# Optimization experiments

Measured on AMD Instinct MI355X. Metric: run time of the kernel, lower is better.

## Reference

```python
import jax, jax.numpy as jnp
import numpy as np

NUM_LAYERS = 3


def setup_inputs() -> dict:
    key = jax.random.key(0)
    k1, k2 = jax.random.split(key)
    N = 200000          # num_users + num_items
    D = 64              # latent_dim
    E = 4000000         # number of directed edges
    edge_index = jax.random.randint(k1, (2, E), 0, N, dtype=jnp.int64)
    emb_weight = 0.1 * jax.random.normal(k2, (N, D), dtype=jnp.float32)  # nn.init.normal_(std=0.1)
    return {"edge_index": edge_index, "emb_weight": emb_weight}


def reference(edge_index, emb_weight):
    N, D = emb_weight.shape
    src, dst = edge_index[0], edge_index[1]
    # gcn_norm (no self loops), as used by LGConv
    deg = jax.ops.segment_sum(jnp.ones_like(src, dtype=emb_weight.dtype), dst, num_segments=N)
    dinv = jnp.where(deg > 0, jax.lax.rsqrt(jnp.maximum(deg, 1.0)), 0.0)
    norm = dinv[src] * dinv[dst]            # [E]
    emb0 = emb_weight
    emb = emb0
    acc = emb0                              # running sum over layer embeddings
    for _ in range(NUM_LAYERS):
        msgs = norm[:, None] * emb[src]     # [E, D] irregular gather
        emb = jax.ops.segment_sum(msgs, dst, num_segments=N)  # scatter-add aggregate
        acc = acc + emb
    out = acc / (NUM_LAYERS + 1)            # mean over stacked layer embeddings
    return (emb0, out)
```

## Files before the change

kernel.cpp:

```cpp
#include <hip/hip_runtime.h>
#include <hip/hip_fp16.h>

#define DIM 64
#define BNODE_SHIFT 8
#define BNODE (1 << BNODE_SHIFT)
#define MAXNB 1024
#define BCAP_SHIFT 13
#define BCAP (1 << BCAP_SHIFT)
#define BIN_CHUNK 4096

__device__ inline __half2 as_h2(unsigned int u) {
    union { unsigned int u; __half2 h; } x; x.u = u; return x.h;
}
__device__ inline unsigned int as_u32(__half2 h) {
    union { unsigned int u; __half2 h; } x; x.h = h; return x.u;
}

__global__ void init_cursor_kernel(int* __restrict__ cursor, int NB) {
    int b = blockIdx.x * blockDim.x + threadIdx.x;
    if (b < NB) cursor[b] = b << BCAP_SHIFT;
}

__global__ void bin_kernel(const int* __restrict__ src, const int* __restrict__ dst,
                           int* __restrict__ cursor, unsigned int* __restrict__ packed,
                           int E, int NB) {
    __shared__ int lhist[MAXNB];
    __shared__ int lbase[MAXNB];
    const int t = threadIdx.x;
    for (int i = t; i < MAXNB; i += blockDim.x) lhist[i] = 0;
    __syncthreads();
    const long long beg = (long long)blockIdx.x * BIN_CHUNK;
    for (int j = 0; j < BIN_CHUNK / 256; ++j) {
        long long idx = beg + j * 256 + t;
        if (idx < E) atomicAdd(&lhist[dst[idx] >> BNODE_SHIFT], 1);
    }
    __syncthreads();
    for (int b = t; b < NB; b += blockDim.x) {
        int c = lhist[b];
        lbase[b] = c ? atomicAdd(&cursor[b], c) : 0;
    }
    __syncthreads();
    for (int i = t; i < MAXNB; i += blockDim.x) lhist[i] = 0;
    __syncthreads();
    for (int j = 0; j < BIN_CHUNK / 256; ++j) {
        long long idx = beg + j * 256 + t;
        if (idx < E) {
            int d = dst[idx];
            int b = d >> BNODE_SHIFT;
            int lpos = atomicAdd(&lhist[b], 1);
            packed[lbase[b] + lpos] =
                (unsigned int)src[idx] | ((unsigned int)(d & (BNODE - 1)) << 18);
        }
    }
}

__global__ void __launch_bounds__(BNODE) csr_kernel(
        const int* __restrict__ cursor, const unsigned int* __restrict__ packed,
        int* __restrict__ csr_src, float* __restrict__ dinv,
        int4* __restrict__ desc, int N) {
    __shared__ int hist[BNODE];
    __shared__ int s[BNODE];
    const int t = threadIdx.x;
    const int b = blockIdx.x;
    const int b0 = b << BCAP_SHIFT;
    const int cnt = cursor[b] - b0;
    hist[t] = 0;
    __syncthreads();
    for (int i = t; i < cnt; i += BNODE)
        atomicAdd(&hist[packed[b0 + i] >> 18], 1);
    __syncthreads();
    s[t] = hist[t];
    __syncthreads();
    for (int off = 1; off < BNODE; off <<= 1) {
        int v = s[t];
        int a = (t >= off) ? s[t - off] : 0;
        __syncthreads();
        s[t] = v + a;
        __syncthreads();
    }
    const int deg = hist[t];
    const int excl = s[t] - deg;
    const int myBeg = b0 + excl;
    const int node = (b << BNODE_SHIFT) + t;
    if (node < N) {
        float fd = (float)deg;
        float di2 = deg > 0 ? 1.0f / fd : 0.0f;
        dinv[node] = deg > 0 ? rsqrtf(fd) : 0.0f;
        desc[node] = make_int4(myBeg, myBeg + deg, deg, __float_as_int(di2));
    }
    __syncthreads();
    s[t] = excl;
    __syncthreads();
    for (int i = t; i < cnt; i += BNODE) {
        unsigned int p = packed[b0 + i];
        int lpos = atomicAdd(&s[p >> 18], 1);
        csr_src[b0 + lpos] = (int)(p & 0x3FFFFu);
    }
}

__global__ void conv0_kernel(const float* __restrict__ emb0, const float* __restrict__ dinv,
                             float* __restrict__ out_emb0, unsigned int* __restrict__ S0,
                             int n4) {
    int i = blockIdx.x * blockDim.x + threadIdx.x;
    if (i >= n4) return;
    float4 v = ((const float4*)emb0)[i];
    ((float4*)out_emb0)[i] = v;
    float w = dinv[i >> 4];
    uint2 o;
    o.x = as_u32(__float22half2_rn(make_float2(w * v.x, w * v.y)));
    o.y = as_u32(__float22half2_rn(make_float2(w * v.z, w * v.w)));
    ((uint2*)S0)[i] = o;
}

template<bool LAST>
__global__ void gather_kernel(const int4* __restrict__ desc,
                              const int* __restrict__ csr_src,
                              const unsigned int* __restrict__ S_in,
                              unsigned int* __restrict__ S_out,
                              const unsigned int* __restrict__ S1,
                              const float* __restrict__ emb0,
                              float* __restrict__ acc,
                              int N) {
    const int node = (blockIdx.x * blockDim.x + threadIdx.x) >> 6;
    if (node >= N) return;
    const int lane = threadIdx.x & 63;
    const int eg = lane >> 3;
    const int q  = lane & 7;
    const int4 d = desc[node];
    const int end = d.y;
    __half2 a0 = as_h2(0u), a1 = as_h2(0u), a2 = as_h2(0u), a3 = as_h2(0u);
    int i = d.x + eg;
    for (; i + 8 < end; i += 16) {
        int s0 = csr_src[i];
        int s1 = csr_src[i + 8];
        uint4 g0 = *(const uint4*)(S_in + (size_t)s0 * (DIM / 2) + q * 4);
        uint4 g1 = *(const uint4*)(S_in + (size_t)s1 * (DIM / 2) + q * 4);
        a0 = __hadd2(a0, as_h2(g0.x)); a1 = __hadd2(a1, as_h2(g0.y));
        a2 = __hadd2(a2, as_h2(g0.z)); a3 = __hadd2(a3, as_h2(g0.w));
        a0 = __hadd2(a0, as_h2(g1.x)); a1 = __hadd2(a1, as_h2(g1.y));
        a2 = __hadd2(a2, as_h2(g1.z)); a3 = __hadd2(a3, as_h2(g1.w));
    }
    if (i < end) {
        int s0 = csr_src[i];
        uint4 g0 = *(const uint4*)(S_in + (size_t)s0 * (DIM / 2) + q * 4);
        a0 = __hadd2(a0, as_h2(g0.x)); a1 = __hadd2(a1, as_h2(g0.y));
        a2 = __hadd2(a2, as_h2(g0.z)); a3 = __hadd2(a3, as_h2(g0.w));
    }
    #pragma unroll
    for (int m = 8; m < 64; m <<= 1) {
        a0 = __hadd2(a0, as_h2(__shfl_xor(as_u32(a0), m, 64)));
        a1 = __hadd2(a1, as_h2(__shfl_xor(as_u32(a1), m, 64)));
        a2 = __hadd2(a2, as_h2(__shfl_xor(as_u32(a2), m, 64)));
        a3 = __hadd2(a3, as_h2(__shfl_xor(as_u32(a3), m, 64)));
    }
    if (lane >= 8) return;
    const float di2 = __int_as_float(d.w);
    float2 f0 = __half22float2(a0);
    float2 f1 = __half22float2(a1);
    float2 f2 = __half22float2(a2);
    float2 f3 = __half22float2(a3);
    if (!LAST) {
        uint4 o;
        o.x = as_u32(__float22half2_rn(make_float2(di2 * f0.x, di2 * f0.y)));
        o.y = as_u32(__float22half2_rn(make_float2(di2 * f1.x, di2 * f1.y)));
        o.z = as_u32(__float22half2_rn(make_float2(di2 * f2.x, di2 * f2.y)));
        o.w = as_u32(__float22half2_rn(make_float2(di2 * f3.x, di2 * f3.y)));
        *(uint4*)(S_out + (size_t)node * (DIM / 2) + lane * 4) = o;
    } else {
        float rs = di2 > 0.f ? rsqrtf(di2) : 0.f;
        float dv = sqrtf(di2);
        uint4 u1 = *(const uint4*)(S1   + (size_t)node * (DIM / 2) + lane * 4);
        uint4 u2 = *(const uint4*)(S_in + (size_t)node * (DIM / 2) + lane * 4);
        float2 b0 = __half22float2(as_h2(u1.x)), c0 = __half22float2(as_h2(u2.x));
        float2 b1 = __half22float2(as_h2(u1.y)), c1 = __half22float2(as_h2(u2.y));
        float2 b2 = __half22float2(as_h2(u1.z)), c2 = __half22float2(as_h2(u2.z));
        float2 b3 = __half22float2(as_h2(u1.w)), c3 = __half22float2(as_h2(u2.w));
        const float* e = emb0 + (size_t)node * DIM + lane * 8;
        float4 e0 = *(const float4*)(e);
        float4 e1 = *(const float4*)(e + 4);
        float4 o0, o1;
        o0.x = 0.25f * (e0.x + rs * (b0.x + c0.x) + dv * f0.x);
        o0.y = 0.25f * (e0.y + rs * (b0.y + c0.y) + dv * f0.y);
        o0.z = 0.25f * (e0.z + rs * (b1.x + c1.x) + dv * f1.x);
        o0.w = 0.25f * (e0.w + rs * (b1.y + c1.y) + dv * f1.y);
        o1.x = 0.25f * (e1.x + rs * (b2.x + c2.x) + dv * f2.x);
        o1.y = 0.25f * (e1.y + rs * (b2.y + c2.y) + dv * f2.y);
        o1.z = 0.25f * (e1.z + rs * (b3.x + c3.x) + dv * f3.x);
        o1.w = 0.25f * (e1.w + rs * (b3.y + c3.y) + dv * f3.y);
        float* ap = acc + (size_t)node * DIM + lane * 8;
        *(float4*)(ap) = o0;
        *(float4*)(ap + 4) = o1;
    }
}

static inline size_t align256(size_t x) { return (x + 255) & ~(size_t)255; }

extern "C" void kernel_launch(void* const* d_in, const int* in_sizes, int n_in,
                              void* d_out, int out_size, void* d_ws, size_t ws_size,
                              hipStream_t stream) {
    const int*   edge = (const int*)d_in[0];
    const float* emb0 = (const float*)d_in[1];
    const int E = in_sizes[0] / 2;
    const int N = in_sizes[1] / DIM;
    const int* src = edge;
    const int* dst = edge + E;
    const int NB = (N + BNODE - 1) >> BNODE_SHIFT;

    char* ws = (char*)d_ws;
    int* cursor        = (int*)ws;  ws += align256((size_t)(MAXNB + 1) * sizeof(int));
    float* dinv        = (float*)ws; ws += align256((size_t)N * sizeof(float));
    int4* desc         = (int4*)ws; ws += align256((size_t)N * sizeof(int4));
    unsigned int* packed = (unsigned int*)ws; ws += align256((size_t)NB * BCAP * sizeof(int));
    int* csr_src       = (int*)ws;  ws += align256((size_t)NB * BCAP * sizeof(int));
    unsigned int* SX   = (unsigned int*)ws; ws += align256((size_t)N * (DIM / 2) * sizeof(unsigned int));
    unsigned int* SY   = (unsigned int*)ws; ws += align256((size_t)N * (DIM / 2) * sizeof(unsigned int));

    float* out_emb0 = (float*)d_out;
    float* acc      = out_emb0 + (size_t)N * DIM;

    const int blocks_e = (int)(((long long)E + BIN_CHUNK - 1) / BIN_CHUNK);
    const int n4 = N * DIM / 4;

    init_cursor_kernel<<<(NB + 255) / 256, 256, 0, stream>>>(cursor, NB);
    bin_kernel<<<blocks_e, 256, 0, stream>>>(src, dst, cursor, packed, E, NB);
    csr_kernel<<<NB, BNODE, 0, stream>>>(cursor, packed, csr_src, dinv, desc, N);

    conv0_kernel<<<(n4 + 255) / 256, 256, 0, stream>>>(emb0, dinv, out_emb0, SX, n4);

    const long long gthreads = (long long)N * 64;
    const int ggrid = (int)((gthreads + 255) / 256);
    gather_kernel<false><<<ggrid, 256, 0, stream>>>(desc, csr_src, SX, SY, nullptr, nullptr, nullptr, N);
    gather_kernel<false><<<ggrid, 256, 0, stream>>>(desc, csr_src, SY, SX, nullptr, nullptr, nullptr, N);
    gather_kernel<true><<<ggrid, 256, 0, stream>>>(desc, csr_src, SX, nullptr, SY, emb0, acc, N);
}
```

Measured before the change: 534.3 us.

## Replace two-level bucketed CSR build with global atomic histogram, scan, and scatter

Swaps the bucket-binning CSR construction (LDS histograms per chunk, packed intermediate, per-bucket local sort) for a direct approach. It builds a global atomic degree histogram, runs a two-level prefix scan, then scatters edges with global atomics on per-node cursors. This drops the packed intermediate buffer and the second pass over the binned data. In exchange, every edge now issues global atomics to random addresses twice, and edges within a node's CSR segment come out in nondeterministic order, which loses the locality the bucketed writes had.

```diff
diff --git a/kernel.cpp b/kernel.cpp
--- a/kernel.cpp
+++ b/kernel.cpp
@@ -2,12 +2,6 @@
 #include <hip/hip_fp16.h>
 
 #define DIM 64
-#define BNODE_SHIFT 8
-#define BNODE (1 << BNODE_SHIFT)
-#define MAXNB 1024
-#define BCAP_SHIFT 13
-#define BCAP (1 << BCAP_SHIFT)
-#define BIN_CHUNK 4096
 
 __device__ inline __half2 as_h2(unsigned int u) {
     union { unsigned int u; __half2 h; } x; x.u = u; return x.h;
@@ -16,86 +10,84 @@
     union { unsigned int u; __half2 h; } x; x.h = h; return x.u;
 }
 
-__global__ void init_cursor_kernel(int* __restrict__ cursor, int NB) {
-    int b = blockIdx.x * blockDim.x + threadIdx.x;
-    if (b < NB) cursor[b] = b << BCAP_SHIFT;
-}
-
-__global__ void bin_kernel(const int* __restrict__ src, const int* __restrict__ dst,
-                           int* __restrict__ cursor, unsigned int* __restrict__ packed,
-                           int E, int NB) {
-    __shared__ int lhist[MAXNB];
-    __shared__ int lbase[MAXNB];
+__global__ void zero_deg_kernel(int* __restrict__ deg, int N) {
+    int i = blockIdx.x * blockDim.x + threadIdx.x;
+    if (i < N) deg[i] = 0;
+}
+
+__global__ void hist_kernel(const int* __restrict__ dst, int* __restrict__ deg, int E) {
+    int i = blockIdx.x * blockDim.x + threadIdx.x;
+    if (i < E) atomicAdd(&deg[dst[i]], 1);
+}
+
+__global__ void scan_partial_kernel(const int* __restrict__ deg, int* __restrict__ tmpoff,
+                                    int* __restrict__ bsum, int N) {
+    __shared__ int s[256];
     const int t = threadIdx.x;
-    for (int i = t; i < MAXNB; i += blockDim.x) lhist[i] = 0;
+    const int base = (blockIdx.x << 11) + (t << 3);
+    int v[8];
+    int sum = 0;
+    #pragma unroll
+    for (int k = 0; k < 8; ++k) {
+        int node = base + k;
+        int d = (node < N) ? deg[node] : 0;
+        v[k] = sum;
+        sum += d;
+    }
+    s[t] = sum;
     __syncthreads();
-    const long long beg = (long long)blockIdx.x * BIN_CHUNK;
-    for (int j = 0; j < BIN_CHUNK / 256; ++j) {
-        long long idx = beg + j * 256 + t;
-        if (idx < E) atomicAdd(&lhist[dst[idx] >> BNODE_SHIFT], 1);
-    }
+    for (int off = 1; off < 256; off <<= 1) {
+        int x = s[t];
+        int a = (t >= off) ? s[t - off] : 0;
+        __syncthreads();
+        s[t] = x + a;
+        __syncthreads();
+    }
+    const int excl = s[t] - sum;
+    #pragma unroll
+    for (int k = 0; k < 8; ++k) {
+        int node = base + k;
+        if (node < N) tmpoff[node] = excl + v[k];
+    }
+    if (t == 255) bsum[blockIdx.x] = s[255];
+}
+
+__global__ void scan_blocks_kernel(int* __restrict__ bsum, int NBL) {
+    __shared__ int s[128];
+    const int t = threadIdx.x;
+    int v = (t < NBL) ? bsum[t] : 0;
+    s[t] = v;
     __syncthreads();
-    for (int b = t; b < NB; b += blockDim.x) {
-        int c = lhist[b];
-        lbase[b] = c ? atomicAdd(&cursor[b], c) : 0;
-    }
-    __syncthreads();
-    for (int i = t; i < MAXNB; i += blockDim.x) lhist[i] = 0;
-    __syncthreads();
-    for (int j = 0; j < BIN_CHUNK / 256; ++j) {
-        long long idx = beg + j * 256 + t;
-        if (idx < E) {
-            int d = dst[idx];
-            int b = d >> BNODE_SHIFT;
-            int lpos = atomicAdd(&lhist[b], 1);
-            packed[lbase[b] + lpos] =
-                (unsigned int)src[idx] | ((unsigned int)(d & (BNODE - 1)) << 18);
-        }
-    }
-}
-
-__global__ void __launch_bounds__(BNODE) csr_kernel(
-        const int* __restrict__ cursor, const unsigned int* __restrict__ packed,
-        int* __restrict__ csr_src, float* __restrict__ dinv,
-        int4* __restrict__ desc, int N) {
-    __shared__ int hist[BNODE];
-    __shared__ int s[BNODE];
-    const int t = threadIdx.x;
-    const int b = blockIdx.x;
-    const int b0 = b << BCAP_SHIFT;
-    const int cnt = cursor[b] - b0;
-    hist[t] = 0;
-    __syncthreads();
-    for (int i = t; i < cnt; i += BNODE)
-        atomicAdd(&hist[packed[b0 + i] >> 18], 1);
-    __syncthreads();
-    s[t] = hist[t];
-    __syncthreads();
-    for (int off = 1; off < BNODE; off <<= 1) {
-        int v = s[t];
+    for (int off = 1; off < 128; off <<= 1) {
+        int x = s[t];
         int a = (t >= off) ? s[t - off] : 0;
         __syncthreads();
-        s[t] = v + a;
-        __syncthreads();
-    }
-    const int deg = hist[t];
-    const int excl = s[t] - deg;
-    const int myBeg = b0 + excl;
-    const int node = (b << BNODE_SHIFT) + t;
-    if (node < N) {
-        float fd = (float)deg;
-        float di2 = deg > 0 ? 1.0f / fd : 0.0f;
-        dinv[node] = deg > 0 ? rsqrtf(fd) : 0.0f;
-        desc[node] = make_int4(myBeg, myBeg + deg, deg, __float_as_int(di2));
-    }
-    __syncthreads();
-    s[t] = excl;
-    __syncthreads();
-    for (int i = t; i < cnt; i += BNODE) {
-        unsigned int p = packed[b0 + i];
-        int lpos = atomicAdd(&s[p >> 18], 1);
-        csr_src[b0 + lpos] = (int)(p & 0x3FFFFu);
-    }
+        s[t] = x + a;
+        __syncthreads();
+    }
+    if (t < NBL) bsum[t] = s[t] - v;
+}
+
+__global__ void apply_kernel(const int* __restrict__ deg, const int* __restrict__ tmpoff,
+                             const int* __restrict__ bsum, int4* __restrict__ desc,
+                             float* __restrict__ dinv, int* __restrict__ cur, int N) {
+    int node = blockIdx.x * blockDim.x + threadIdx.x;
+    if (node >= N) return;
+    int beg = bsum[node >> 11] + tmpoff[node];
+    int dg = deg[node];
+    float fd = (float)dg;
+    float di2 = dg > 0 ? 1.0f / fd : 0.0f;
+    dinv[node] = dg > 0 ? rsqrtf(fd) : 0.0f;
+    desc[node] = make_int4(beg, beg + dg, dg, __float_as_int(di2));
+    cur[node] = beg;
+}
+
+__global__ void scatter_kernel(const int* __restrict__ src, const int* __restrict__ dst,
+                               int* __restrict__ cur, int* __restrict__ csr_src, int E) {
+    int i = blockIdx.x * blockDim.x + threadIdx.x;
+    if (i >= E) return;
+    int pos = atomicAdd(&cur[dst[i]], 1);
+    csr_src[pos] = src[i];
 }
 
 __global__ void conv0_kernel(const float* __restrict__ emb0, const float* __restrict__ dinv,
@@ -204,26 +196,32 @@
     const int N = in_sizes[1] / DIM;
     const int* src = edge;
     const int* dst = edge + E;
-    const int NB = (N + BNODE - 1) >> BNODE_SHIFT;
 
     char* ws = (char*)d_ws;
-    int* cursor        = (int*)ws;  ws += align256((size_t)(MAXNB + 1) * sizeof(int));
-    float* dinv        = (float*)ws; ws += align256((size_t)N * sizeof(float));
-    int4* desc         = (int4*)ws; ws += align256((size_t)N * sizeof(int4));
-    unsigned int* packed = (unsigned int*)ws; ws += align256((size_t)NB * BCAP * sizeof(int));
-    int* csr_src       = (int*)ws;  ws += align256((size_t)NB * BCAP * sizeof(int));
-    unsigned int* SX   = (unsigned int*)ws; ws += align256((size_t)N * (DIM / 2) * sizeof(unsigned int));
-    unsigned int* SY   = (unsigned int*)ws; ws += align256((size_t)N * (DIM / 2) * sizeof(unsigned int));
+    int* deg        = (int*)ws;  ws += align256((size_t)N * sizeof(int));
+    int* cur        = (int*)ws;  ws += align256((size_t)N * sizeof(int));
+    int* tmpoff     = (int*)ws;  ws += align256((size_t)N * sizeof(int));
+    int* bsum       = (int*)ws;  ws += align256(256 * sizeof(int));
+    float* dinv     = (float*)ws; ws += align256((size_t)N * sizeof(float));
+    int4* desc      = (int4*)ws; ws += align256((size_t)N * sizeof(int4));
+    int* csr_src    = (int*)ws;  ws += align256((size_t)E * sizeof(int));
+    unsigned int* SX = (unsigned int*)ws; ws += align256((size_t)N * (DIM / 2) * sizeof(unsigned int));
+    unsigned int* SY = (unsigned int*)ws; ws += align256((size_t)N * (DIM / 2) * sizeof(unsigned int));
 
     float* out_emb0 = (float*)d_out;
     float* acc      = out_emb0 + (size_t)N * DIM;
 
-    const int blocks_e = (int)(((long long)E + BIN_CHUNK - 1) / BIN_CHUNK);
     const int n4 = N * DIM / 4;
-
-    init_cursor_kernel<<<(NB + 255) / 256, 256, 0, stream>>>(cursor, NB);
-    bin_kernel<<<blocks_e, 256, 0, stream>>>(src, dst, cursor, packed, E, NB);
-    csr_kernel<<<NB, BNODE, 0, stream>>>(cursor, packed, csr_src, dinv, desc, N);
+    const int NBL = (N + 2047) >> 11;
+    const int eblocks = (E + 255) / 256;
+    const int nblocks = (N + 255) / 256;
+
+    zero_deg_kernel<<<nblocks, 256, 0, stream>>>(deg, N);
+    hist_kernel<<<eblocks, 256, 0, stream>>>(dst, deg, E);
+    scan_partial_kernel<<<NBL, 256, 0, stream>>>(deg, tmpoff, bsum, N);
+    scan_blocks_kernel<<<1, 128, 0, stream>>>(bsum, NBL);
+    apply_kernel<<<nblocks, 256, 0, stream>>>(deg, tmpoff, bsum, desc, dinv, cur, N);
+    scatter_kernel<<<eblocks, 256, 0, stream>>>(src, dst, cur, csr_src, E);
 
     conv0_kernel<<<(n4 + 255) / 256, 256, 0, stream>>>(emb0, dinv, out_emb0, SX, n4);
 
```

New measurement: 894.1 us. +67.3%, slower.
